# Kernel tuning notes

Measured on AMD Instinct MI355X. Metric: run time of the kernel, lower is better.

The kernel has to match this reference:

```python
import jax, jax.numpy as jnp
import numpy as np

B, N, M, C, H = 256, 4096, 64, 512, 4
IN, OUT = 64, 64
EPS = 1e-8

def setup_inputs():
    key = jax.random.key(0)
    ks = jax.random.split(key, 8)
    def w(k, shape, scale=0.05):
        return jax.random.normal(k, shape, dtype=jnp.float32) * scale
    return {
        "in_data": jax.random.normal(ks[0], (B, IN), dtype=jnp.float32),
        "memory": jax.random.normal(ks[1], (B, N, M), dtype=jnp.float32),
        "h0": jnp.zeros((B, C), jnp.float32),
        "c0": jnp.zeros((B, C), jnp.float32),
        "prev_weights": jnp.zeros((2 * H, B, N), jnp.float32),
        "prev_reads": jax.random.normal(ks[2], (H, B, M), dtype=jnp.float32),
        "W_ih": w(ks[3], (4 * C, IN + H * M)),
        "b_ih": jnp.zeros((4 * C,), jnp.float32),
        "W_hh": w(ks[4], (4 * C, C)),
        "b_hh": jnp.zeros((4 * C,), jnp.float32),
        "W_out": w(ks[5], (OUT, C + H * M)),
        "b_out": jnp.zeros((OUT,), jnp.float32),
        "W_addr": w(ks[6], (2 * H, M + 6, C)),
        "b_addr": jnp.zeros((2 * H, M + 6), jnp.float32),
        "W_ea": w(ks[7], (H, 2 * M, C)),
        "b_ea": jnp.zeros((H, 2 * M), jnp.float32),
    }


def reference(in_data, memory, h0, c0, prev_weights, prev_reads,
              W_ih, b_ih, W_hh, b_hh, W_out, b_out,
              W_addr, b_addr, W_ea, b_ea):
    # ---- controller: LSTMCell over [input, prev_reads...] ----
    x = jnp.concatenate([in_data] + [prev_reads[i] for i in range(H)], axis=-1)  # [B, IN+H*M]
    gates = x @ W_ih.T + b_ih + h0 @ W_hh.T + b_hh                               # [B, 4C]
    i_g, f_g, g_g, o_g = jnp.split(gates, 4, axis=-1)
    c = jax.nn.sigmoid(f_g) * c0 + jax.nn.sigmoid(i_g) * jnp.tanh(g_g)
    h = jax.nn.sigmoid(o_g) * jnp.tanh(c)

    # ---- heads: alternate read / write, sequential over memory ----
    mem = memory
    reads = []
    for hi in range(2 * H):
        p = c @ W_addr[hi].T + b_addr[hi]                     # [B, M+6]
        k = jnp.tanh(p[:, :M])                                # key
        beta = jax.nn.softplus(p[:, M:M + 1])                 # key strength
        gate = jax.nn.sigmoid(p[:, M + 1:M + 2])              # interpolation gate
        s = jax.nn.softmax(p[:, M + 2:M + 5], axis=-1)        # shift weights (3)
        gamma = 1.0 + jax.nn.softplus(p[:, M + 5:M + 6])      # sharpening
        # content addressing: cosine similarity against all memory rows
        dot = jnp.einsum('bnm,bm->bn', mem, k)                # [B, N]
        norms = jnp.linalg.norm(mem, axis=-1) * jnp.linalg.norm(k, axis=-1, keepdims=True)
        wc = jax.nn.softmax(beta * dot / (norms + EPS), axis=-1)
        # interpolation with previous weights
        wg = gate * wc + (1.0 - gate) * prev_weights[hi]
        # circular shift convolution (shifts -1, 0, +1)
        ws = (s[:, 0:1] * jnp.roll(wg, 1, axis=-1)
              + s[:, 1:2] * wg
              + s[:, 2:3] * jnp.roll(wg, -1, axis=-1))
        # sharpening
        wp = ws ** gamma
        w = wp / (jnp.sum(wp, axis=-1, keepdims=True) + EPS)
        if hi % 2 == 0:  # read head
            reads.append(jnp.einsum('bn,bnm->bm', w, mem))
        else:            # write head: erase then add
            ea = c @ W_ea[hi // 2].T + b_ea[hi // 2]          # [B, 2M]
            e = jax.nn.sigmoid(ea[:, :M])
            a = jnp.tanh(ea[:, M:])
            mem = mem * (1.0 - w[:, :, None] * e[:, None, :]) + w[:, :, None] * a[:, None, :]

    # ---- output layer over [h, reads...] ----
    state = jnp.concatenate([h] + reads, axis=-1)             # [B, C+H*M]
    return jax.nn.sigmoid(state @ W_out.T + b_out)            # [B, OUT]
```

## Files before the change

### kernel.cpp

```cpp
#include <hip/hip_runtime.h>
#include <hip/hip_fp16.h>
#include <math.h>

#define EPSF 1e-8f
#define NN 4096
#define BB 256
#define PH ((size_t)BB * NN)

__device__ __forceinline__ float sigf(float x) { return 1.0f / (1.0f + expf(-x)); }
__device__ __forceinline__ float softplusf(float x) { return x > 20.0f ? x : log1pf(expf(x)); }
__device__ __forceinline__ float dot4(float4 a, float4 b) {
  return a.x * b.x + a.y * b.y + a.z * b.z + a.w * b.w;
}
__device__ __forceinline__ unsigned short f2bf(float x) {
  unsigned int u = __float_as_uint(x);
  unsigned int r = (u + 0x7FFF + ((u >> 16) & 1)) >> 16;
  return (unsigned short)r;
}
__device__ __forceinline__ float bf2f(unsigned int lo16) {
  return __uint_as_float(lo16 << 16);
}

__device__ __forceinline__ float gather_x(const float* __restrict__ in_data,
                                          const float* __restrict__ prev_reads,
                                          const float* __restrict__ h0,
                                          int row, int k) {
  if (k < 64) return in_data[row * 64 + k];
  if (k < 320) { int i = (k - 64) >> 6, m = (k - 64) & 63; return prev_reads[((size_t)i * 256 + row) * 64 + m]; }
  return h0[row * 512 + (k - 320)];
}

__global__ __launch_bounds__(256) void gemm_gates_kernel(
    const float* __restrict__ in_data, const float* __restrict__ prev_reads,
    const float* __restrict__ h0, const float* __restrict__ W_ih,
    const float* __restrict__ W_hh, const float* __restrict__ b_ih,
    const float* __restrict__ b_hh, float* __restrict__ gates) {
  __shared__ float As[16][33];
  __shared__ float Ws[16][65];
  int tid = threadIdx.x, tx = tid & 15, ty = tid >> 4;
  int row0 = blockIdx.y * 32, col0 = blockIdx.x * 64;
  float acc[2][4] = {{0,0,0,0},{0,0,0,0}};
  for (int k0 = 0; k0 < 832; k0 += 16) {
    const float* Wp; int kw, KW;
    if (k0 < 320) { Wp = W_ih; kw = k0; KW = 320; }
    else          { Wp = W_hh; kw = k0 - 320; KW = 512; }
    for (int i = tid; i < 32 * 16; i += 256) {
      int rr = i >> 4, cc = i & 15;
      As[cc][rr] = gather_x(in_data, prev_reads, h0, row0 + rr, k0 + cc);
    }
    for (int i = tid; i < 64 * 16; i += 256) {
      int rr = i >> 4, cc = i & 15;
      Ws[cc][rr] = Wp[(size_t)(col0 + rr) * KW + kw + cc];
    }
    __syncthreads();
#pragma unroll
    for (int kk = 0; kk < 16; kk++) {
      float a0 = As[kk][ty * 2 + 0], a1 = As[kk][ty * 2 + 1];
      float w0 = Ws[kk][tx * 4 + 0], w1 = Ws[kk][tx * 4 + 1];
      float w2 = Ws[kk][tx * 4 + 2], w3 = Ws[kk][tx * 4 + 3];
      acc[0][0] += a0 * w0; acc[0][1] += a0 * w1; acc[0][2] += a0 * w2; acc[0][3] += a0 * w3;
      acc[1][0] += a1 * w0; acc[1][1] += a1 * w1; acc[1][2] += a1 * w2; acc[1][3] += a1 * w3;
    }
    __syncthreads();
  }
  for (int i = 0; i < 2; i++)
    for (int j = 0; j < 4; j++) {
      int cc = col0 + tx * 4 + j;
      gates[(size_t)(row0 + ty * 2 + i) * 2048 + cc] = acc[i][j] + b_ih[cc] + b_hh[cc];
    }
}

__global__ void lstm_elem_kernel(const float* __restrict__ gates,
                                 const float* __restrict__ c0,
                                 float* __restrict__ c, float* __restrict__ h) {
  int idx = blockIdx.x * 256 + threadIdx.x;
  if (idx >= 256 * 512) return;
  int b = idx >> 9, u = idx & 511;
  const float* g = gates + (size_t)b * 2048;
  float ig = sigf(g[u]), fg = sigf(g[512 + u]);
  float gg = tanhf(g[1024 + u]), og = sigf(g[1536 + u]);
  float cv = fg * c0[idx] + ig * gg;
  c[idx] = cv;
  h[idx] = og * tanhf(cv);
}

__global__ __launch_bounds__(256) void gemm_heads_kernel(
    const float* __restrict__ C, const float* __restrict__ W_addr,
    const float* __restrict__ W_ea, const float* __restrict__ b_addr,
    const float* __restrict__ b_ea, float* __restrict__ p_raw) {
  __shared__ float As[16][33];
  __shared__ float Ws[16][65];
  int tid = threadIdx.x, tx = tid & 15, ty = tid >> 4;
  int row0 = blockIdx.y * 32, col0 = blockIdx.x * 64;
  float acc[2][4] = {{0,0,0,0},{0,0,0,0}};
  for (int k0 = 0; k0 < 512; k0 += 16) {
    for (int i = tid; i < 32 * 16; i += 256) {
      int rr = i >> 4, cc = i & 15;
      As[cc][rr] = C[(size_t)(row0 + rr) * 512 + k0 + cc];
    }
    for (int i = tid; i < 64 * 16; i += 256) {
      int rr = i >> 4, cc = i & 15;
      int col = col0 + rr;
      float v = 0.f;
      if (col < 560) v = W_addr[(size_t)col * 512 + k0 + cc];
      else if (col < 1072) v = W_ea[(size_t)(col - 560) * 512 + k0 + cc];
      Ws[cc][rr] = v;
    }
    __syncthreads();
#pragma unroll
    for (int kk = 0; kk < 16; kk++) {
      float a0 = As[kk][ty * 2 + 0], a1 = As[kk][ty * 2 + 1];
      float w0 = Ws[kk][tx * 4 + 0], w1 = Ws[kk][tx * 4 + 1];
      float w2 = Ws[kk][tx * 4 + 2], w3 = Ws[kk][tx * 4 + 3];
      acc[0][0] += a0 * w0; acc[0][1] += a0 * w1; acc[0][2] += a0 * w2; acc[0][3] += a0 * w3;
      acc[1][0] += a1 * w0; acc[1][1] += a1 * w1; acc[1][2] += a1 * w2; acc[1][3] += a1 * w3;
    }
    __syncthreads();
  }
  for (int i = 0; i < 2; i++)
    for (int j = 0; j < 4; j++) {
      int col = col0 + tx * 4 + j;
      if (col < 1072) {
        float bias = col < 560 ? b_addr[col] : b_ea[col - 560];
        p_raw[(size_t)(row0 + ty * 2 + i) * 1072 + col] = acc[i][j] + bias;
      }
    }
}

__global__ void params_kernel(const float* __restrict__ p_raw,
    float* __restrict__ knorm, float* __restrict__ betav,
    float* __restrict__ gatev, float* __restrict__ sv,
    float* __restrict__ gammav, float* __restrict__ combo,
    float* __restrict__ scal) {
  int b = blockIdx.x, m = threadIdx.x;
  const float* p = p_raw + (size_t)b * 1072;
  float kv[7];
#pragma unroll
  for (int hi = 0; hi < 7; hi++) {
    float k = tanhf(p[hi * 70 + m]);
    kv[hi] = k;
    float s = k * k;
#pragma unroll
    for (int d = 1; d < 64; d <<= 1) s += __shfl_xor(s, d);
    if (m == 0) {
      int hb = hi * BB + b;
      knorm[hb] = sqrtf(s);
      betav[hb] = softplusf(p[hi * 70 + 64]);
      gatev[hb] = sigf(p[hi * 70 + 65]);
      float a0 = p[hi * 70 + 66], a1 = p[hi * 70 + 67], a2 = p[hi * 70 + 68];
      float mm = fmaxf(a0, fmaxf(a1, a2));
      float e0 = expf(a0 - mm), e1 = expf(a1 - mm), e2 = expf(a2 - mm);
      float es = e0 + e1 + e2;
      sv[hb * 3 + 0] = e0 / es; sv[hb * 3 + 1] = e1 / es; sv[hb * 3 + 2] = e2 / es;
      gammav[hb] = 1.0f + softplusf(p[hi * 70 + 69]);
    }
  }
  float e1 = sigf(p[560 + 0 * 128 + m]),  a1v = tanhf(p[560 + 0 * 128 + 64 + m]);
  float e3 = sigf(p[560 + 1 * 128 + m]),  a3v = tanhf(p[560 + 1 * 128 + 64 + m]);
  float e5 = sigf(p[560 + 2 * 128 + m]),  a5v = tanhf(p[560 + 2 * 128 + 64 + m]);
  size_t bm = (size_t)b * 64 + m;
  combo[0 * 16384 + bm] = kv[0];  combo[1 * 16384 + bm] = kv[1];
  combo[2 * 16384 + bm] = kv[2];  combo[3 * 16384 + bm] = e1 * kv[2];
  combo[4 * 16384 + bm] = kv[3];  combo[5 * 16384 + bm] = e1 * kv[3];
  combo[6 * 16384 + bm] = a1v;    combo[7 * 16384 + bm] = e1 * a1v;
  combo[8 * 16384 + bm] = e1;     combo[9 * 16384 + bm] = e1 * e1;
  combo[10 * 16384 + bm] = kv[4]; combo[11 * 16384 + bm] = kv[5];
  combo[12 * 16384 + bm] = kv[6]; combo[13 * 16384 + bm] = e5 * kv[6];
  combo[14 * 16384 + bm] = a5v;   combo[15 * 16384 + bm] = e5 * a5v;
  combo[16 * 16384 + bm] = e5;    combo[17 * 16384 + bm] = e5 * e5;
  combo[18 * 16384 + bm] = e3;    combo[19 * 16384 + bm] = a3v;
  float s0 = a1v * kv[2], s1 = a1v * kv[3], s2 = a1v * a1v, s3 = a5v * kv[6], s4 = a5v * a5v;
#pragma unroll
  for (int d = 1; d < 64; d <<= 1) {
    s0 += __shfl_xor(s0, d); s1 += __shfl_xor(s1, d); s2 += __shfl_xor(s2, d);
    s3 += __shfl_xor(s3, d); s4 += __shfl_xor(s4, d);
  }
  if (m == 0) {
    scal[b * 8 + 0] = s0; scal[b * 8 + 1] = s1; scal[b * 8 + 2] = s2;
    scal[b * 8 + 3] = s3; scal[b * 8 + 4] = s4;
  }
}

#define CL(j, q) (*(const float4*)(cb + (j) * 64 + (q) * 4))

__global__ __launch_bounds__(256) void phase1_kernel(
    const float* __restrict__ mem, const float* __restrict__ combo,
    const float* __restrict__ scal, const float* __restrict__ knorm,
    const float* __restrict__ betav, unsigned short* __restrict__ mem_bf,
    __half* __restrict__ P) {
  __shared__ float cb[640];
  __shared__ float4 tile[128 * 16];
  int b = blockIdx.y, tid = threadIdx.x;
  for (int i = tid; i < 640; i += 256)
    cb[i] = combo[(size_t)(i >> 6) * 16384 + b * 64 + (i & 63)];
  int n0 = blockIdx.x * 128;
  size_t bo = (size_t)b * NN;
  const float4* src = (const float4*)mem + (bo + n0) * 16;
  ushort4* dst = (ushort4*)mem_bf + (bo + n0) * 16;
#pragma unroll
  for (int i = 0; i < 8; i++) {
    int idx = tid + i * 256;
    float4 v = src[idx];
    int r = idx >> 4, q = idx & 15;
    tile[r * 16 + (q ^ (r & 15))] = v;
    ushort4 o;
    o.x = f2bf(v.x); o.y = f2bf(v.y); o.z = f2bf(v.z); o.w = f2bf(v.w);
    dst[idx] = o;
  }
  __syncthreads();
  float kn0 = knorm[b], be0 = betav[b];
  float kn1 = knorm[BB + b], be1 = betav[BB + b];
  float cak2 = scal[b * 8 + 0], cak3 = scal[b * 8 + 1], caa1 = scal[b * 8 + 2];
  int row = tid >> 1, half = tid & 1;
  float a[11];
#pragma unroll
  for (int k = 0; k < 11; k++) a[k] = 0.f;
#pragma unroll
  for (int j = 0; j < 8; j++) {
    int q = half * 8 + j;
    float4 v = tile[row * 16 + (q ^ (row & 15))];
    float4 sq = make_float4(v.x * v.x, v.y * v.y, v.z * v.z, v.w * v.w);
    a[0] += dot4(v, CL(0, q)); a[1] += dot4(v, CL(1, q));
    a[2] += dot4(v, CL(2, q)); a[3] += dot4(v, CL(3, q));
    a[4] += dot4(v, CL(4, q)); a[5] += dot4(v, CL(5, q));
    a[6] += dot4(v, CL(6, q)); a[7] += dot4(v, CL(7, q));
    a[8] += sq.x + sq.y + sq.z + sq.w;
    a[9] += dot4(sq, CL(8, q)); a[10] += dot4(sq, CL(9, q));
  }
#pragma unroll
  for (int k = 0; k < 11; k++) a[k] += __shfl_xor(a[k], 1);
  if (half == 0) {
    int n = n0 + row;
    float rn = sqrtf(a[8]);
    P[0 * PH + bo + n] = __float2half(be0 * a[0] / (rn * kn0 + EPSF));
    P[1 * PH + bo + n] = __float2half(be1 * a[1] / (rn * kn1 + EPSF));
    P[2 * PH + bo + n] = __float2half(a[2]);
    P[3 * PH + bo + n] = __float2half(a[3] - cak2);
    P[4 * PH + bo + n] = __float2half(a[4]);
    P[5 * PH + bo + n] = __float2half(a[5] - cak3);
    P[6 * PH + bo + n] = __float2half(a[8]);
    P[7 * PH + bo + n] = __float2half(a[9] - a[6]);
    P[8 * PH + bo + n] = __float2half(a[10] - 2.f * a[7] + caa1);
  }
}

__global__ __launch_bounds__(512) void chain_kernel(
    const __half* __restrict__ P, __half* __restrict__ w_g,
    const float* __restrict__ knorm, const float* __restrict__ betav,
    const float* __restrict__ gatev, const float* __restrict__ sv,
    const float* __restrict__ gammav, const float* __restrict__ prev_w,
    int group) {
  __shared__ float wg[NN];
  __shared__ float red[24];
  int b = blockIdx.x, hy = blockIdx.y, tid = threadIdx.x;
  int lane = tid & 63, wv = tid >> 6;
  int head, u_head = 0;
  const __half *SC = nullptr, *Da = nullptr, *Dbc = nullptr;
  const __half *S0p = nullptr, *T1p = nullptr, *T2p = nullptr;
  if (group == 0)      { head = hy;     SC = P + (size_t)hy * PH; }
  else if (group == 1) { head = 2 + hy; Da = P + (size_t)(2 + 2 * hy) * PH; Dbc = P + (size_t)(3 + 2 * hy) * PH;
                         S0p = P + 6 * PH; T1p = P + 7 * PH; T2p = P + 8 * PH; u_head = 1; }
  else if (group == 2) { head = 4 + hy; SC = P + (size_t)hy * PH; }
  else                 { head = 6;      Da = P + 2 * PH; Dbc = P + 3 * PH;
                         S0p = P + 4 * PH; T1p = P + 5 * PH; T2p = P + 6 * PH; u_head = 5; }
  int hb = head * BB + b;
  float kn = knorm[hb], be = betav[hb], ga = gatev[hb], gm = gammav[hb];
  float s0 = sv[hb * 3 + 0], s1 = sv[hb * 3 + 1], s2 = sv[hb * 3 + 2];
  size_t bo = (size_t)b * NN;
  const float* pw = prev_w + (size_t)head * PH + bo;
  const __half* ug = w_g + ((size_t)u_head * BB + b) * NN;
  __half* wout = w_g + ((size_t)head * BB + b) * NN;
  float sc[8];
  float mx = -1e30f;
#pragma unroll
  for (int i = 0; i < 8; i++) {
    int n = tid + i * 512;
    float scv;
    if (SC != nullptr) {
      scv = __half2float(SC[bo + n]);
    } else {
      float u = __half2float(ug[n]);
      float d = __half2float(Da[bo + n]) - u * __half2float(Dbc[bo + n]);
      float nn2 = __half2float(S0p[bo + n]) - 2.f * u * __half2float(T1p[bo + n])
                + u * u * __half2float(T2p[bo + n]);
      nn2 = fmaxf(nn2, 0.f);
      scv = be * d / (sqrtf(nn2) * kn + EPSF);
    }
    sc[i] = scv; mx = fmaxf(mx, scv);
  }
#pragma unroll
  for (int m = 1; m < 64; m <<= 1) mx = fmaxf(mx, __shfl_xor(mx, m));
  if (lane == 0) red[wv] = mx;
  __syncthreads();
  mx = red[0];
#pragma unroll
  for (int w = 1; w < 8; w++) mx = fmaxf(mx, red[w]);
  float sum = 0.f;
#pragma unroll
  for (int i = 0; i < 8; i++) { sc[i] = expf(sc[i] - mx); sum += sc[i]; }
#pragma unroll
  for (int m = 1; m < 64; m <<= 1) sum += __shfl_xor(sum, m);
  if (lane == 0) red[8 + wv] = sum;
  __syncthreads();
  sum = 0.f;
#pragma unroll
  for (int w = 0; w < 8; w++) sum += red[8 + w];
  float inv = 1.0f / sum;
#pragma unroll
  for (int i = 0; i < 8; i++) {
    int n = tid + i * 512;
    wg[n] = ga * (sc[i] * inv) + (1.f - ga) * pw[n];
  }
  __syncthreads();
  float wp[8];
  float sum2 = 0.f;
#pragma unroll
  for (int i = 0; i < 8; i++) {
    int n = tid + i * 512;
    float wsv = s0 * wg[(n + NN - 1) & (NN - 1)] + s1 * wg[n] + s2 * wg[(n + 1) & (NN - 1)];
    wp[i] = powf(wsv, gm);
    sum2 += wp[i];
  }
#pragma unroll
  for (int m = 1; m < 64; m <<= 1) sum2 += __shfl_xor(sum2, m);
  if (lane == 0) red[16 + wv] = sum2;
  __syncthreads();
  sum2 = 0.f;
#pragma unroll
  for (int w = 0; w < 8; w++) sum2 += red[16 + w];
  float invs = 1.0f / (sum2 + EPSF);
#pragma unroll
  for (int i = 0; i < 8; i++) {
    int n = tid + i * 512;
    wout[n] = __float2half(wp[i] * invs);
  }
}

__global__ __launch_bounds__(256) void phase2_kernel(
    const unsigned short* __restrict__ mem_bf, const float* __restrict__ combo,
    const float* __restrict__ scal, const float* __restrict__ knorm,
    const float* __restrict__ betav, const __half* __restrict__ w_g,
    __half* __restrict__ P) {
  __shared__ float cb[1280];
  __shared__ uint4 tileb[128 * 8];
  int b = blockIdx.y, tid = threadIdx.x;
  for (int i = tid; i < 1280; i += 256)
    cb[i] = combo[(size_t)(i >> 6) * 16384 + b * 64 + (i & 63)];
  int n0 = blockIdx.x * 128;
  size_t bo = (size_t)b * NN;
  const uint4* src = (const uint4*)mem_bf + (bo + n0) * 8;
#pragma unroll
  for (int i = 0; i < 4; i++) {
    int idx = tid + i * 256;
    uint4 u = src[idx];
    int r = idx >> 3, g = idx & 7;
    tileb[r * 8 + (g ^ (r & 7))] = u;
  }
  __syncthreads();
  float kn4 = knorm[4 * BB + b], be4 = betav[4 * BB + b];
  float kn5 = knorm[5 * BB + b], be5 = betav[5 * BB + b];
  float cak6 = scal[b * 8 + 3], caa5 = scal[b * 8 + 4];
  int row = tid >> 1, half = tid & 1;
  int n = n0 + row;
  float u1 = __half2float(w_g[((size_t)1 * BB + b) * NN + n]);
  float u3 = __half2float(w_g[((size_t)3 * BB + b) * NN + n]);
  float t[9];
#pragma unroll
  for (int k = 0; k < 9; k++) t[k] = 0.f;
#pragma unroll
  for (int j = 0; j < 4; j++) {
    int g = half * 4 + j;
    uint4 uv = tileb[row * 8 + (g ^ (row & 7))];
#pragma unroll
    for (int h = 0; h < 2; h++) {
      unsigned int pa = h ? uv.z : uv.x;
      unsigned int pb = h ? uv.w : uv.y;
      float4 v;
      v.x = bf2f(pa & 0xFFFFu); v.y = bf2f(pa >> 16);
      v.z = bf2f(pb & 0xFFFFu); v.w = bf2f(pb >> 16);
      int q = g * 2 + h;
      float4 e1v = CL(8, q), a1v = CL(6, q), e3v = CL(18, q), a3v = CL(19, q);
      float4 m1, m2;
      m1.x = v.x * (1.f - u1 * e1v.x) + u1 * a1v.x;
      m1.y = v.y * (1.f - u1 * e1v.y) + u1 * a1v.y;
      m1.z = v.z * (1.f - u1 * e1v.z) + u1 * a1v.z;
      m1.w = v.w * (1.f - u1 * e1v.w) + u1 * a1v.w;
      m2.x = m1.x * (1.f - u3 * e3v.x) + u3 * a3v.x;
      m2.y = m1.y * (1.f - u3 * e3v.y) + u3 * a3v.y;
      m2.z = m1.z * (1.f - u3 * e3v.z) + u3 * a3v.z;
      m2.w = m1.w * (1.f - u3 * e3v.w) + u3 * a3v.w;
      float4 sq = make_float4(m2.x * m2.x, m2.y * m2.y, m2.z * m2.z, m2.w * m2.w);
      t[0] += dot4(m2, CL(10, q)); t[1] += dot4(m2, CL(11, q));
      t[2] += dot4(m2, CL(12, q)); t[3] += dot4(m2, CL(13, q));
      t[4] += dot4(m2, CL(14, q)); t[5] += dot4(m2, CL(15, q));
      t[6] += sq.x + sq.y + sq.z + sq.w;
      t[7] += dot4(sq, CL(16, q)); t[8] += dot4(sq, CL(17, q));
    }
  }
#pragma unroll
  for (int k = 0; k < 9; k++) t[k] += __shfl_xor(t[k], 1);
  if (half == 0) {
    float rn = sqrtf(t[6]);
    P[0 * PH + bo + n] = __float2half(be4 * t[0] / (rn * kn4 + EPSF));
    P[1 * PH + bo + n] = __float2half(be5 * t[1] / (rn * kn5 + EPSF));
    P[2 * PH + bo + n] = __float2half(t[2]);
    P[3 * PH + bo + n] = __float2half(t[3] - cak6);
    P[4 * PH + bo + n] = __float2half(t[6]);
    P[5 * PH + bo + n] = __float2half(t[7] - t[4]);
    P[6 * PH + bo + n] = __float2half(t[8] - 2.f * t[5] + caa5);
  }
}

__global__ __launch_bounds__(256) void phase3_kernel(
    const unsigned short* __restrict__ mem_bf, const float* __restrict__ combo,
    const __half* __restrict__ w_g, float* __restrict__ reads) {
  __shared__ float cb[1280];
  __shared__ __half ws[7 * 512];
  __shared__ float sred[4 * 4 * 16 * 4];
  int b = blockIdx.y, chunk = blockIdx.x, tid = threadIdx.x;
  for (int i = tid; i < 1280; i += 256)
    cb[i] = combo[(size_t)(i >> 6) * 16384 + b * 64 + (i & 63)];
  int nbase = chunk * 512;
  for (int i = tid; i < 7 * 512; i += 256) {
    int hh = i >> 9, nn = i & 511;
    ws[i] = w_g[((size_t)hh * BB + b) * NN + nbase + nn];
  }
  __syncthreads();
  int wv = tid >> 6, lane = tid & 63, q = lane & 15, rl = lane >> 4;
  float4 e1v = CL(8, q), a1v = CL(6, q), e3v = CL(18, q), a3v = CL(19, q);
  float4 e5v = CL(16, q), a5v = CL(14, q);
  size_t bo = (size_t)b * NN;
  const ushort4* mbr = (const ushort4*)mem_bf + bo * 16;
  float A[4][4];
#pragma unroll
  for (int j = 0; j < 4; j++)
#pragma unroll
    for (int cmp = 0; cmp < 4; cmp++) A[j][cmp] = 0.f;
#pragma unroll 4
  for (int t = 0; t < 32; t++) {
    int nl = t * 16 + wv * 4 + rl;
    int n = nbase + nl;
    ushort4 uv = mbr[(size_t)n * 16 + q];
    float vx = bf2f(uv.x), vy = bf2f(uv.y), vz = bf2f(uv.z), vw = bf2f(uv.w);
    float w0v = __half2float(ws[0 * 512 + nl]);
    float u1  = __half2float(ws[1 * 512 + nl]);
    float w2v = __half2float(ws[2 * 512 + nl]);
    float u3  = __half2float(ws[3 * 512 + nl]);
    float w4v = __half2float(ws[4 * 512 + nl]);
    float u5  = __half2float(ws[5 * 512 + nl]);
    float w6v = __half2float(ws[6 * 512 + nl]);
    A[0][0] += w0v * vx; A[0][1] += w0v * vy; A[0][2] += w0v * vz; A[0][3] += w0v * vw;
    float m1x = vx * (1.f - u1 * e1v.x) + u1 * a1v.x;
    float m1y = vy * (1.f - u1 * e1v.y) + u1 * a1v.y;
    float m1z = vz * (1.f - u1 * e1v.z) + u1 * a1v.z;
    float m1w = vw * (1.f - u1 * e1v.w) + u1 * a1v.w;
    A[1][0] += w2v * m1x; A[1][1] += w2v * m1y; A[1][2] += w2v * m1z; A[1][3] += w2v * m1w;
    float m2x = m1x * (1.f - u3 * e3v.x) + u3 * a3v.x;
    float m2y = m1y * (1.f - u3 * e3v.y) + u3 * a3v.y;
    float m2z = m1z * (1.f - u3 * e3v.z) + u3 * a3v.z;
    float m2w = m1w * (1.f - u3 * e3v.w) + u3 * a3v.w;
    A[2][0] += w4v * m2x; A[2][1] += w4v * m2y; A[2][2] += w4v * m2z; A[2][3] += w4v * m2w;
    float m3x = m2x * (1.f - u5 * e5v.x) + u5 * a5v.x;
    float m3y = m2y * (1.f - u5 * e5v.y) + u5 * a5v.y;
    float m3z = m2z * (1.f - u5 * e5v.z) + u5 * a5v.z;
    float m3w = m2w * (1.f - u5 * e5v.w) + u5 * a5v.w;
    A[3][0] += w6v * m3x; A[3][1] += w6v * m3y; A[3][2] += w6v * m3z; A[3][3] += w6v * m3w;
  }
#pragma unroll
  for (int j = 0; j < 4; j++)
#pragma unroll
    for (int cmp = 0; cmp < 4; cmp++) {
      float x = A[j][cmp];
      x += __shfl_xor(x, 16);
      x += __shfl_xor(x, 32);
      A[j][cmp] = x;
    }
  if (rl == 0)
#pragma unroll
    for (int j = 0; j < 4; j++)
#pragma unroll
      for (int cmp = 0; cmp < 4; cmp++)
        sred[((j * 4 + wv) * 16 + q) * 4 + cmp] = A[j][cmp];
  __syncthreads();
  if (tid < 256) {
    int j = tid >> 6, qq = (tid >> 2) & 15, cc = tid & 3;
    float s = 0.f;
#pragma unroll
    for (int w = 0; w < 4; w++) s += sred[((j * 4 + w) * 16 + qq) * 4 + cc];
    atomicAdd(&reads[(size_t)j * 16384 + b * 64 + qq * 4 + cc], s);
  }
}

__global__ __launch_bounds__(256) void gemm_out_kernel(
    const float* __restrict__ h, const float* __restrict__ reads,
    const float* __restrict__ W_out, const float* __restrict__ b_out,
    float* __restrict__ out) {
  __shared__ float As[16][33];
  __shared__ float Ws[16][65];
  int tid = threadIdx.x, tx = tid & 15, ty = tid >> 4;
  int row0 = blockIdx.y * 32;
  float acc[2][4] = {{0,0,0,0},{0,0,0,0}};
  for (int k0 = 0; k0 < 768; k0 += 16) {
    for (int i = tid; i < 32 * 16; i += 256) {
      int rr = i >> 4, cc = i & 15;
      int row = row0 + rr, k = k0 + cc;
      float v;
      if (k < 512) v = h[row * 512 + k];
      else { int slot = (k - 512) >> 6, m = (k - 512) & 63; v = reads[((size_t)slot * 256 + row) * 64 + m]; }
      As[cc][rr] = v;
    }
    for (int i = tid; i < 64 * 16; i += 256) {
      int rr = i >> 4, cc = i & 15;
      Ws[cc][rr] = W_out[(size_t)rr * 768 + k0 + cc];
    }
    __syncthreads();
#pragma unroll
    for (int kk = 0; kk < 16; kk++) {
      float a0 = As[kk][ty * 2 + 0], a1 = As[kk][ty * 2 + 1];
      float w0 = Ws[kk][tx * 4 + 0], w1 = Ws[kk][tx * 4 + 1];
      float w2 = Ws[kk][tx * 4 + 2], w3 = Ws[kk][tx * 4 + 3];
      acc[0][0] += a0 * w0; acc[0][1] += a0 * w1; acc[0][2] += a0 * w2; acc[0][3] += a0 * w3;
      acc[1][0] += a1 * w0; acc[1][1] += a1 * w1; acc[1][2] += a1 * w2; acc[1][3] += a1 * w3;
    }
    __syncthreads();
  }
  for (int i = 0; i < 2; i++)
    for (int j = 0; j < 4; j++) {
      int cc = tx * 4 + j;
      out[(size_t)(row0 + ty * 2 + i) * 64 + cc] = sigf(acc[i][j] + b_out[cc]);
    }
}

extern "C" void kernel_launch(void* const* d_in, const int* in_sizes, int n_in,
                              void* d_out, int out_size, void* d_ws, size_t ws_size,
                              hipStream_t stream) {
  const float* in_data = (const float*)d_in[0];
  const float* memory  = (const float*)d_in[1];
  const float* h0      = (const float*)d_in[2];
  const float* c0      = (const float*)d_in[3];
  const float* prev_w  = (const float*)d_in[4];
  const float* prev_r  = (const float*)d_in[5];
  const float* W_ih    = (const float*)d_in[6];
  const float* b_ih    = (const float*)d_in[7];
  const float* W_hh    = (const float*)d_in[8];
  const float* b_hh    = (const float*)d_in[9];
  const float* W_out   = (const float*)d_in[10];
  const float* b_out   = (const float*)d_in[11];
  const float* W_addr  = (const float*)d_in[12];
  const float* b_addr  = (const float*)d_in[13];
  const float* W_ea    = (const float*)d_in[14];
  const float* b_ea    = (const float*)d_in[15];
  float* out = (float*)d_out;
  (void)in_sizes; (void)n_in; (void)out_size; (void)ws_size;

  float* ws = (float*)d_ws;
  size_t off = 0;
  auto alloc = [&](size_t n) { float* p = ws + off; off += (n + 63) & ~(size_t)63; return p; };
  float* gates  = alloc(256 * 2048);
  float* cbuf   = alloc(256 * 512);
  float* hbuf   = alloc(256 * 512);
  float* p_raw  = alloc(256 * 1072);
  float* knorm  = alloc(8 * 256);
  float* betav  = alloc(8 * 256);
  float* gatev  = alloc(8 * 256);
  float* sv     = alloc(8 * 256 * 3);
  float* gammav = alloc(8 * 256);
  float* combo  = alloc(20 * 16384);
  float* scal   = alloc(256 * 8);
  __half* P     = (__half*)alloc(9 * PH / 2);
  float* reads  = alloc(4 * 16384);
  unsigned short* mem_bf = (unsigned short*)alloc(33554432);
  __half* w_g   = (__half*)alloc(7 * BB * NN / 2);

  gemm_gates_kernel<<<dim3(32, 8), 256, 0, stream>>>(in_data, prev_r, h0, W_ih, W_hh, b_ih, b_hh, gates);
  lstm_elem_kernel<<<(256 * 512 + 255) / 256, 256, 0, stream>>>(gates, c0, cbuf, hbuf);
  gemm_heads_kernel<<<dim3(17, 8), 256, 0, stream>>>(cbuf, W_addr, W_ea, b_addr, b_ea, p_raw);
  params_kernel<<<256, 64, 0, stream>>>(p_raw, knorm, betav, gatev, sv, gammav, combo, scal);
  hipMemsetAsync(reads, 0, 4 * 16384 * sizeof(float), stream);

  phase1_kernel<<<dim3(32, 256), 256, 0, stream>>>(memory, combo, scal, knorm, betav, mem_bf, P);
  chain_kernel<<<dim3(256, 2), 512, 0, stream>>>(P, w_g, knorm, betav, gatev, sv, gammav, prev_w, 0);
  chain_kernel<<<dim3(256, 2), 512, 0, stream>>>(P, w_g, knorm, betav, gatev, sv, gammav, prev_w, 1);
  phase2_kernel<<<dim3(32, 256), 256, 0, stream>>>(mem_bf, combo, scal, knorm, betav, w_g, P);
  chain_kernel<<<dim3(256, 2), 512, 0, stream>>>(P, w_g, knorm, betav, gatev, sv, gammav, prev_w, 2);
  chain_kernel<<<dim3(256, 1), 512, 0, stream>>>(P, w_g, knorm, betav, gatev, sv, gammav, prev_w, 3);
  phase3_kernel<<<dim3(8, 256), 256, 0, stream>>>(mem_bf, combo, w_g, reads);

  gemm_out_kernel<<<dim3(1, 8), 256, 0, stream>>>(hbuf, reads, W_out, b_out, out);
}
```

Before: 888.1 us.

## Merge front-end and chain kernels using software grid barriers

Fuses the gate GEMM, LSTM elementwise, heads GEMM and params stages into one persistent 256-block kernel. Pairs of chain kernels are merged into two kernels separated by atomic grid-wide barriers, which removes several launch gaps. Also switches expf/powf to the fast __expf/__powf intrinsics in the chain. The barriers assume all blocks are co-resident and can deadlock otherwise; the chain23 second stage idles half the blocks, and the fast intrinsics are slightly less accurate.

```diff
diff --git a/kernel.cpp b/kernel.cpp
--- a/kernel.cpp
+++ b/kernel.cpp
@@ -19,6 +19,21 @@
 }
 __device__ __forceinline__ float bf2f(unsigned int lo16) {
   return __uint_as_float(lo16 << 16);
+}
+
+__device__ __forceinline__ void gbar(unsigned* arr, unsigned* rel, unsigned nb, unsigned call) {
+  __syncthreads();
+  if (threadIdx.x == 0) {
+    unsigned old = __hip_atomic_fetch_add(arr, 1u, __ATOMIC_ACQ_REL, __HIP_MEMORY_SCOPE_AGENT);
+    if (old == call * nb - 1u) {
+      __hip_atomic_store(rel, call, __ATOMIC_RELEASE, __HIP_MEMORY_SCOPE_AGENT);
+    } else {
+      while (__hip_atomic_load(rel, __ATOMIC_ACQUIRE, __HIP_MEMORY_SCOPE_AGENT) < call) {
+        __builtin_amdgcn_s_sleep(2);
+      }
+    }
+  }
+  __syncthreads();
 }
 
 __device__ __forceinline__ float gather_x(const float* __restrict__ in_data,
@@ -30,154 +45,159 @@
   return h0[row * 512 + (k - 320)];
 }
 
-__global__ __launch_bounds__(256) void gemm_gates_kernel(
+__global__ __launch_bounds__(256) void front_kernel(
     const float* __restrict__ in_data, const float* __restrict__ prev_reads,
-    const float* __restrict__ h0, const float* __restrict__ W_ih,
-    const float* __restrict__ W_hh, const float* __restrict__ b_ih,
-    const float* __restrict__ b_hh, float* __restrict__ gates) {
-  __shared__ float As[16][33];
-  __shared__ float Ws[16][65];
-  int tid = threadIdx.x, tx = tid & 15, ty = tid >> 4;
-  int row0 = blockIdx.y * 32, col0 = blockIdx.x * 64;
-  float acc[2][4] = {{0,0,0,0},{0,0,0,0}};
-  for (int k0 = 0; k0 < 832; k0 += 16) {
-    const float* Wp; int kw, KW;
-    if (k0 < 320) { Wp = W_ih; kw = k0; KW = 320; }
-    else          { Wp = W_hh; kw = k0 - 320; KW = 512; }
-    for (int i = tid; i < 32 * 16; i += 256) {
-      int rr = i >> 4, cc = i & 15;
-      As[cc][rr] = gather_x(in_data, prev_reads, h0, row0 + rr, k0 + cc);
-    }
-    for (int i = tid; i < 64 * 16; i += 256) {
-      int rr = i >> 4, cc = i & 15;
-      Ws[cc][rr] = Wp[(size_t)(col0 + rr) * KW + kw + cc];
-    }
-    __syncthreads();
-#pragma unroll
-    for (int kk = 0; kk < 16; kk++) {
-      float a0 = As[kk][ty * 2 + 0], a1 = As[kk][ty * 2 + 1];
-      float w0 = Ws[kk][tx * 4 + 0], w1 = Ws[kk][tx * 4 + 1];
-      float w2 = Ws[kk][tx * 4 + 2], w3 = Ws[kk][tx * 4 + 3];
-      acc[0][0] += a0 * w0; acc[0][1] += a0 * w1; acc[0][2] += a0 * w2; acc[0][3] += a0 * w3;
-      acc[1][0] += a1 * w0; acc[1][1] += a1 * w1; acc[1][2] += a1 * w2; acc[1][3] += a1 * w3;
-    }
-    __syncthreads();
-  }
-  for (int i = 0; i < 2; i++)
-    for (int j = 0; j < 4; j++) {
-      int cc = col0 + tx * 4 + j;
-      gates[(size_t)(row0 + ty * 2 + i) * 2048 + cc] = acc[i][j] + b_ih[cc] + b_hh[cc];
-    }
-}
-
-__global__ void lstm_elem_kernel(const float* __restrict__ gates,
-                                 const float* __restrict__ c0,
-                                 float* __restrict__ c, float* __restrict__ h) {
-  int idx = blockIdx.x * 256 + threadIdx.x;
-  if (idx >= 256 * 512) return;
-  int b = idx >> 9, u = idx & 511;
-  const float* g = gates + (size_t)b * 2048;
-  float ig = sigf(g[u]), fg = sigf(g[512 + u]);
-  float gg = tanhf(g[1024 + u]), og = sigf(g[1536 + u]);
-  float cv = fg * c0[idx] + ig * gg;
-  c[idx] = cv;
-  h[idx] = og * tanhf(cv);
-}
-
-__global__ __launch_bounds__(256) void gemm_heads_kernel(
-    const float* __restrict__ C, const float* __restrict__ W_addr,
-    const float* __restrict__ W_ea, const float* __restrict__ b_addr,
-    const float* __restrict__ b_ea, float* __restrict__ p_raw) {
-  __shared__ float As[16][33];
-  __shared__ float Ws[16][65];
-  int tid = threadIdx.x, tx = tid & 15, ty = tid >> 4;
-  int row0 = blockIdx.y * 32, col0 = blockIdx.x * 64;
-  float acc[2][4] = {{0,0,0,0},{0,0,0,0}};
-  for (int k0 = 0; k0 < 512; k0 += 16) {
-    for (int i = tid; i < 32 * 16; i += 256) {
-      int rr = i >> 4, cc = i & 15;
-      As[cc][rr] = C[(size_t)(row0 + rr) * 512 + k0 + cc];
-    }
-    for (int i = tid; i < 64 * 16; i += 256) {
-      int rr = i >> 4, cc = i & 15;
-      int col = col0 + rr;
-      float v = 0.f;
-      if (col < 560) v = W_addr[(size_t)col * 512 + k0 + cc];
-      else if (col < 1072) v = W_ea[(size_t)(col - 560) * 512 + k0 + cc];
-      Ws[cc][rr] = v;
-    }
-    __syncthreads();
-#pragma unroll
-    for (int kk = 0; kk < 16; kk++) {
-      float a0 = As[kk][ty * 2 + 0], a1 = As[kk][ty * 2 + 1];
-      float w0 = Ws[kk][tx * 4 + 0], w1 = Ws[kk][tx * 4 + 1];
-      float w2 = Ws[kk][tx * 4 + 2], w3 = Ws[kk][tx * 4 + 3];
-      acc[0][0] += a0 * w0; acc[0][1] += a0 * w1; acc[0][2] += a0 * w2; acc[0][3] += a0 * w3;
-      acc[1][0] += a1 * w0; acc[1][1] += a1 * w1; acc[1][2] += a1 * w2; acc[1][3] += a1 * w3;
-    }
-    __syncthreads();
-  }
-  for (int i = 0; i < 2; i++)
-    for (int j = 0; j < 4; j++) {
-      int col = col0 + tx * 4 + j;
-      if (col < 1072) {
-        float bias = col < 560 ? b_addr[col] : b_ea[col - 560];
-        p_raw[(size_t)(row0 + ty * 2 + i) * 1072 + col] = acc[i][j] + bias;
-      }
-    }
-}
-
-__global__ void params_kernel(const float* __restrict__ p_raw,
+    const float* __restrict__ h0, const float* __restrict__ c0,
+    const float* __restrict__ W_ih, const float* __restrict__ W_hh,
+    const float* __restrict__ b_ih, const float* __restrict__ b_hh,
+    const float* __restrict__ W_addr, const float* __restrict__ W_ea,
+    const float* __restrict__ b_addr, const float* __restrict__ b_ea,
+    float* __restrict__ gates, float* __restrict__ cbuf, float* __restrict__ hbuf,
+    float* __restrict__ p_raw,
     float* __restrict__ knorm, float* __restrict__ betav,
     float* __restrict__ gatev, float* __restrict__ sv,
     float* __restrict__ gammav, float* __restrict__ combo,
-    float* __restrict__ scal) {
-  int b = blockIdx.x, m = threadIdx.x;
-  const float* p = p_raw + (size_t)b * 1072;
-  float kv[7];
-#pragma unroll
-  for (int hi = 0; hi < 7; hi++) {
-    float k = tanhf(p[hi * 70 + m]);
-    kv[hi] = k;
-    float s = k * k;
-#pragma unroll
-    for (int d = 1; d < 64; d <<= 1) s += __shfl_xor(s, d);
+    float* __restrict__ scal, unsigned* __restrict__ bars) {
+  __shared__ float As[16][33];
+  __shared__ float Ws[16][65];
+  int tid = threadIdx.x, blk = blockIdx.x;
+  int tx = tid & 15, ty = tid >> 4;
+
+  {
+    int col0 = (blk & 31) * 64, row0 = (blk >> 5) * 32;
+    float acc[2][4] = {{0,0,0,0},{0,0,0,0}};
+    for (int k0 = 0; k0 < 832; k0 += 16) {
+      const float* Wp; int kw, KW;
+      if (k0 < 320) { Wp = W_ih; kw = k0; KW = 320; }
+      else          { Wp = W_hh; kw = k0 - 320; KW = 512; }
+      for (int i = tid; i < 32 * 16; i += 256) {
+        int rr = i >> 4, cc = i & 15;
+        As[cc][rr] = gather_x(in_data, prev_reads, h0, row0 + rr, k0 + cc);
+      }
+      for (int i = tid; i < 64 * 16; i += 256) {
+        int rr = i >> 4, cc = i & 15;
+        Ws[cc][rr] = Wp[(size_t)(col0 + rr) * KW + kw + cc];
+      }
+      __syncthreads();
+#pragma unroll
+      for (int kk = 0; kk < 16; kk++) {
+        float a0 = As[kk][ty * 2 + 0], a1 = As[kk][ty * 2 + 1];
+        float w0 = Ws[kk][tx * 4 + 0], w1 = Ws[kk][tx * 4 + 1];
+        float w2 = Ws[kk][tx * 4 + 2], w3 = Ws[kk][tx * 4 + 3];
+        acc[0][0] += a0 * w0; acc[0][1] += a0 * w1; acc[0][2] += a0 * w2; acc[0][3] += a0 * w3;
+        acc[1][0] += a1 * w0; acc[1][1] += a1 * w1; acc[1][2] += a1 * w2; acc[1][3] += a1 * w3;
+      }
+      __syncthreads();
+    }
+    for (int i = 0; i < 2; i++)
+      for (int j = 0; j < 4; j++) {
+        int cc = col0 + tx * 4 + j;
+        gates[(size_t)(row0 + ty * 2 + i) * 2048 + cc] = acc[i][j] + b_ih[cc] + b_hh[cc];
+      }
+  }
+  gbar(bars + 0, bars + 1, 256, 1);
+
+  {
+#pragma unroll
+    for (int r = 0; r < 2; r++) {
+      int idx = blk * 512 + r * 256 + tid;
+      int b = idx >> 9, u = idx & 511;
+      const float* g = gates + (size_t)b * 2048;
+      float ig = sigf(g[u]), fg = sigf(g[512 + u]);
+      float gg = tanhf(g[1024 + u]), og = sigf(g[1536 + u]);
+      float cv = fg * c0[idx] + ig * gg;
+      cbuf[idx] = cv;
+      hbuf[idx] = og * tanhf(cv);
+    }
+  }
+  gbar(bars + 0, bars + 1, 256, 2);
+
+  if (blk < 136) {
+    int col0 = (blk % 17) * 64, row0 = (blk / 17) * 32;
+    float acc[2][4] = {{0,0,0,0},{0,0,0,0}};
+    for (int k0 = 0; k0 < 512; k0 += 16) {
+      for (int i = tid; i < 32 * 16; i += 256) {
+        int rr = i >> 4, cc = i & 15;
+        As[cc][rr] = cbuf[(size_t)(row0 + rr) * 512 + k0 + cc];
+      }
+      for (int i = tid; i < 64 * 16; i += 256) {
+        int rr = i >> 4, cc = i & 15;
+        int col = col0 + rr;
+        float v = 0.f;
+        if (col < 560) v = W_addr[(size_t)col * 512 + k0 + cc];
+        else if (col < 1072) v = W_ea[(size_t)(col - 560) * 512 + k0 + cc];
+        Ws[cc][rr] = v;
+      }
+      __syncthreads();
+#pragma unroll
+      for (int kk = 0; kk < 16; kk++) {
+        float a0 = As[kk][ty * 2 + 0], a1 = As[kk][ty * 2 + 1];
+        float w0 = Ws[kk][tx * 4 + 0], w1 = Ws[kk][tx * 4 + 1];
+        float w2 = Ws[kk][tx * 4 + 2], w3 = Ws[kk][tx * 4 + 3];
+        acc[0][0] += a0 * w0; acc[0][1] += a0 * w1; acc[0][2] += a0 * w2; acc[0][3] += a0 * w3;
+        acc[1][0] += a1 * w0; acc[1][1] += a1 * w1; acc[1][2] += a1 * w2; acc[1][3] += a1 * w3;
+      }
+      __syncthreads();
+    }
+    for (int i = 0; i < 2; i++)
+      for (int j = 0; j < 4; j++) {
+        int col = col0 + tx * 4 + j;
+        if (col < 1072) {
+          float bias = col < 560 ? b_addr[col] : b_ea[col - 560];
+          p_raw[(size_t)(row0 + ty * 2 + i) * 1072 + col] = acc[i][j] + bias;
+        }
+      }
+  }
+  gbar(bars + 0, bars + 1, 256, 3);
+
+  if (tid < 64) {
+    int b = blk, m = tid;
+    const float* p = p_raw + (size_t)b * 1072;
+    float kv[7];
+#pragma unroll
+    for (int hi = 0; hi < 7; hi++) {
+      float k = tanhf(p[hi * 70 + m]);
+      kv[hi] = k;
+      float s = k * k;
+#pragma unroll
+      for (int d = 1; d < 64; d <<= 1) s += __shfl_xor(s, d);
+      if (m == 0) {
+        int hb = hi * BB + b;
+        knorm[hb] = sqrtf(s);
+        betav[hb] = softplusf(p[hi * 70 + 64]);
+        gatev[hb] = sigf(p[hi * 70 + 65]);
+        float a0 = p[hi * 70 + 66], a1 = p[hi * 70 + 67], a2 = p[hi * 70 + 68];
+        float mm = fmaxf(a0, fmaxf(a1, a2));
+        float e0 = expf(a0 - mm), e1 = expf(a1 - mm), e2 = expf(a2 - mm);
+        float es = e0 + e1 + e2;
+        sv[hb * 3 + 0] = e0 / es; sv[hb * 3 + 1] = e1 / es; sv[hb * 3 + 2] = e2 / es;
+        gammav[hb] = 1.0f + softplusf(p[hi * 70 + 69]);
+      }
+    }
+    float e1 = sigf(p[560 + 0 * 128 + m]),  a1v = tanhf(p[560 + 0 * 128 + 64 + m]);
+    float e3 = sigf(p[560 + 1 * 128 + m]),  a3v = tanhf(p[560 + 1 * 128 + 64 + m]);
+    float e5 = sigf(p[560 + 2 * 128 + m]),  a5v = tanhf(p[560 + 2 * 128 + 64 + m]);
+    size_t bm = (size_t)b * 64 + m;
+    combo[0 * 16384 + bm] = kv[0];  combo[1 * 16384 + bm] = kv[1];
+    combo[2 * 16384 + bm] = kv[2];  combo[3 * 16384 + bm] = e1 * kv[2];
+    combo[4 * 16384 + bm] = kv[3];  combo[5 * 16384 + bm] = e1 * kv[3];
+    combo[6 * 16384 + bm] = a1v;    combo[7 * 16384 + bm] = e1 * a1v;
+    combo[8 * 16384 + bm] = e1;     combo[9 * 16384 + bm] = e1 * e1;
+    combo[10 * 16384 + bm] = kv[4]; combo[11 * 16384 + bm] = kv[5];
+    combo[12 * 16384 + bm] = kv[6]; combo[13 * 16384 + bm] = e5 * kv[6];
+    combo[14 * 16384 + bm] = a5v;   combo[15 * 16384 + bm] = e5 * a5v;
+    combo[16 * 16384 + bm] = e5;    combo[17 * 16384 + bm] = e5 * e5;
+    combo[18 * 16384 + bm] = e3;    combo[19 * 16384 + bm] = a3v;
+    float s0 = a1v * kv[2], s1 = a1v * kv[3], s2 = a1v * a1v, s3 = a5v * kv[6], s4 = a5v * a5v;
+#pragma unroll
+    for (int d = 1; d < 64; d <<= 1) {
+      s0 += __shfl_xor(s0, d); s1 += __shfl_xor(s1, d); s2 += __shfl_xor(s2, d);
+      s3 += __shfl_xor(s3, d); s4 += __shfl_xor(s4, d);
+    }
     if (m == 0) {
-      int hb = hi * BB + b;
-      knorm[hb] = sqrtf(s);
-      betav[hb] = softplusf(p[hi * 70 + 64]);
-      gatev[hb] = sigf(p[hi * 70 + 65]);
-      float a0 = p[hi * 70 + 66], a1 = p[hi * 70 + 67], a2 = p[hi * 70 + 68];
-      float mm = fmaxf(a0, fmaxf(a1, a2));
-      float e0 = expf(a0 - mm), e1 = expf(a1 - mm), e2 = expf(a2 - mm);
-      float es = e0 + e1 + e2;
-      sv[hb * 3 + 0] = e0 / es; sv[hb * 3 + 1] = e1 / es; sv[hb * 3 + 2] = e2 / es;
-      gammav[hb] = 1.0f + softplusf(p[hi * 70 + 69]);
-    }
-  }
-  float e1 = sigf(p[560 + 0 * 128 + m]),  a1v = tanhf(p[560 + 0 * 128 + 64 + m]);
-  float e3 = sigf(p[560 + 1 * 128 + m]),  a3v = tanhf(p[560 + 1 * 128 + 64 + m]);
-  float e5 = sigf(p[560 + 2 * 128 + m]),  a5v = tanhf(p[560 + 2 * 128 + 64 + m]);
-  size_t bm = (size_t)b * 64 + m;
-  combo[0 * 16384 + bm] = kv[0];  combo[1 * 16384 + bm] = kv[1];
-  combo[2 * 16384 + bm] = kv[2];  combo[3 * 16384 + bm] = e1 * kv[2];
-  combo[4 * 16384 + bm] = kv[3];  combo[5 * 16384 + bm] = e1 * kv[3];
-  combo[6 * 16384 + bm] = a1v;    combo[7 * 16384 + bm] = e1 * a1v;
-  combo[8 * 16384 + bm] = e1;     combo[9 * 16384 + bm] = e1 * e1;
-  combo[10 * 16384 + bm] = kv[4]; combo[11 * 16384 + bm] = kv[5];
-  combo[12 * 16384 + bm] = kv[6]; combo[13 * 16384 + bm] = e5 * kv[6];
-  combo[14 * 16384 + bm] = a5v;   combo[15 * 16384 + bm] = e5 * a5v;
-  combo[16 * 16384 + bm] = e5;    combo[17 * 16384 + bm] = e5 * e5;
-  combo[18 * 16384 + bm] = e3;    combo[19 * 16384 + bm] = a3v;
-  float s0 = a1v * kv[2], s1 = a1v * kv[3], s2 = a1v * a1v, s3 = a5v * kv[6], s4 = a5v * a5v;
-#pragma unroll
-  for (int d = 1; d < 64; d <<= 1) {
-    s0 += __shfl_xor(s0, d); s1 += __shfl_xor(s1, d); s2 += __shfl_xor(s2, d);
-    s3 += __shfl_xor(s3, d); s4 += __shfl_xor(s4, d);
-  }
-  if (m == 0) {
-    scal[b * 8 + 0] = s0; scal[b * 8 + 1] = s1; scal[b * 8 + 2] = s2;
-    scal[b * 8 + 3] = s3; scal[b * 8 + 4] = s4;
+      scal[b * 8 + 0] = s0; scal[b * 8 + 1] = s1; scal[b * 8 + 2] = s2;
+      scal[b * 8 + 3] = s3; scal[b * 8 + 4] = s4;
+    }
   }
 }
 
@@ -244,32 +264,21 @@
   }
 }
 
-__global__ __launch_bounds__(512) void chain_kernel(
-    const __half* __restrict__ P, __half* __restrict__ w_g,
+__device__ void chain_core(int tid, int b, int head,
+    const __half* __restrict__ SC, const __half* __restrict__ Da,
+    const __half* __restrict__ Dbc, const __half* __restrict__ S0p,
+    const __half* __restrict__ T1p, const __half* __restrict__ T2p,
+    const __half* __restrict__ ug, __half* __restrict__ wout,
+    float* wg, float* red,
     const float* __restrict__ knorm, const float* __restrict__ betav,
     const float* __restrict__ gatev, const float* __restrict__ sv,
-    const float* __restrict__ gammav, const float* __restrict__ prev_w,
-    int group) {
-  __shared__ float wg[NN];
-  __shared__ float red[24];
-  int b = blockIdx.x, hy = blockIdx.y, tid = threadIdx.x;
+    const float* __restrict__ gammav, const float* __restrict__ prev_w) {
   int lane = tid & 63, wv = tid >> 6;
-  int head, u_head = 0;
-  const __half *SC = nullptr, *Da = nullptr, *Dbc = nullptr;
-  const __half *S0p = nullptr, *T1p = nullptr, *T2p = nullptr;
-  if (group == 0)      { head = hy;     SC = P + (size_t)hy * PH; }
-  else if (group == 1) { head = 2 + hy; Da = P + (size_t)(2 + 2 * hy) * PH; Dbc = P + (size_t)(3 + 2 * hy) * PH;
-                         S0p = P + 6 * PH; T1p = P + 7 * PH; T2p = P + 8 * PH; u_head = 1; }
-  else if (group == 2) { head = 4 + hy; SC = P + (size_t)hy * PH; }
-  else                 { head = 6;      Da = P + 2 * PH; Dbc = P + 3 * PH;
-                         S0p = P + 4 * PH; T1p = P + 5 * PH; T2p = P + 6 * PH; u_head = 5; }
   int hb = head * BB + b;
   float kn = knorm[hb], be = betav[hb], ga = gatev[hb], gm = gammav[hb];
   float s0 = sv[hb * 3 + 0], s1 = sv[hb * 3 + 1], s2 = sv[hb * 3 + 2];
   size_t bo = (size_t)b * NN;
   const float* pw = prev_w + (size_t)head * PH + bo;
-  const __half* ug = w_g + ((size_t)u_head * BB + b) * NN;
-  __half* wout = w_g + ((size_t)head * BB + b) * NN;
   float sc[8];
   float mx = -1e30f;
 #pragma unroll
@@ -297,7 +306,7 @@
   for (int w = 1; w < 8; w++) mx = fmaxf(mx, red[w]);
   float sum = 0.f;
 #pragma unroll
-  for (int i = 0; i < 8; i++) { sc[i] = expf(sc[i] - mx); sum += sc[i]; }
+  for (int i = 0; i < 8; i++) { sc[i] = __expf(sc[i] - mx); sum += sc[i]; }
 #pragma unroll
   for (int m = 1; m < 64; m <<= 1) sum += __shfl_xor(sum, m);
   if (lane == 0) red[8 + wv] = sum;
@@ -318,7 +327,7 @@
   for (int i = 0; i < 8; i++) {
     int n = tid + i * 512;
     float wsv = s0 * wg[(n + NN - 1) & (NN - 1)] + s1 * wg[n] + s2 * wg[(n + 1) & (NN - 1)];
-    wp[i] = powf(wsv, gm);
+    wp[i] = __powf(wsv, gm);
     sum2 += wp[i];
   }
 #pragma unroll
@@ -333,6 +342,48 @@
   for (int i = 0; i < 8; i++) {
     int n = tid + i * 512;
     wout[n] = __float2half(wp[i] * invs);
+  }
+  __syncthreads();
+}
+
+__global__ __launch_bounds__(512) void chains01_kernel(
+    const __half* __restrict__ P, __half* __restrict__ w_g,
+    const float* __restrict__ knorm, const float* __restrict__ betav,
+    const float* __restrict__ gatev, const float* __restrict__ sv,
+    const float* __restrict__ gammav, const float* __restrict__ prev_w,
+    unsigned* __restrict__ bars) {
+  __shared__ float wg[NN];
+  __shared__ float red[24];
+  int b = blockIdx.x, hy = blockIdx.y, tid = threadIdx.x;
+  chain_core(tid, b, hy, P + (size_t)hy * PH, nullptr, nullptr, nullptr, nullptr, nullptr,
+             nullptr, w_g + ((size_t)hy * BB + b) * NN, wg, red,
+             knorm, betav, gatev, sv, gammav, prev_w);
+  gbar(bars + 0, bars + 1, 512, 1);
+  chain_core(tid, b, 2 + hy, nullptr,
+             P + (size_t)(2 + 2 * hy) * PH, P + (size_t)(3 + 2 * hy) * PH,
+             P + 6 * PH, P + 7 * PH, P + 8 * PH,
+             w_g + ((size_t)1 * BB + b) * NN, w_g + ((size_t)(2 + hy) * BB + b) * NN, wg, red,
+             knorm, betav, gatev, sv, gammav, prev_w);
+}
+
+__global__ __launch_bounds__(512) void chains23_kernel(
+    const __half* __restrict__ P, __half* __restrict__ w_g,
+    const float* __restrict__ knorm, const float* __restrict__ betav,
+    const float* __restrict__ gatev, const float* __restrict__ sv,
+    const float* __restrict__ gammav, const float* __restrict__ prev_w,
+    unsigned* __restrict__ bars) {
+  __shared__ float wg[NN];
+  __shared__ float red[24];
+  int b = blockIdx.x, hy = blockIdx.y, tid = threadIdx.x;
+  chain_core(tid, b, 4 + hy, P + (size_t)hy * PH, nullptr, nullptr, nullptr, nullptr, nullptr,
+             nullptr, w_g + ((size_t)(4 + hy) * BB + b) * NN, wg, red,
+             knorm, betav, gatev, sv, gammav, prev_w);
+  gbar(bars + 0, bars + 1, 512, 1);
+  if (hy == 0) {
+    chain_core(tid, b, 6, nullptr, P + 2 * PH, P + 3 * PH,
+               P + 4 * PH, P + 5 * PH, P + 6 * PH,
+               w_g + ((size_t)5 * BB + b) * NN, w_g + ((size_t)6 * BB + b) * NN, wg, red,
+               knorm, betav, gatev, sv, gammav, prev_w);
   }
 }
 
@@ -569,22 +620,21 @@
   float* scal   = alloc(256 * 8);
   __half* P     = (__half*)alloc(9 * PH / 2);
   float* reads  = alloc(4 * 16384);
+  unsigned* bars = (unsigned*)alloc(64);
   unsigned short* mem_bf = (unsigned short*)alloc(33554432);
   __half* w_g   = (__half*)alloc(7 * BB * NN / 2);
 
-  gemm_gates_kernel<<<dim3(32, 8), 256, 0, stream>>>(in_data, prev_r, h0, W_ih, W_hh, b_ih, b_hh, gates);
-  lstm_elem_kernel<<<(256 * 512 + 255) / 256, 256, 0, stream>>>(gates, c0, cbuf, hbuf);
-  gemm_heads_kernel<<<dim3(17, 8), 256, 0, stream>>>(cbuf, W_addr, W_ea, b_addr, b_ea, p_raw);
-  params_kernel<<<256, 64, 0, stream>>>(p_raw, knorm, betav, gatev, sv, gammav, combo, scal);
-  hipMemsetAsync(reads, 0, 4 * 16384 * sizeof(float), stream);
-
+  (void)hipMemsetAsync(reads, 0, (4 * 16384 + 64) * sizeof(float), stream);
+
+  front_kernel<<<256, 256, 0, stream>>>(in_data, prev_r, h0, c0, W_ih, W_hh, b_ih, b_hh,
+                                        W_addr, W_ea, b_addr, b_ea,
+                                        gates, cbuf, hbuf, p_raw,
+                                        knorm, betav, gatev, sv, gammav, combo, scal,
+                                        bars + 0);
   phase1_kernel<<<dim3(32, 256), 256, 0, stream>>>(memory, combo, scal, knorm, betav, mem_bf, P);
-  chain_kernel<<<dim3(256, 2), 512, 0, stream>>>(P, w_g, knorm, betav, gatev, sv, gammav, prev_w, 0);
-  chain_kernel<<<dim3(256, 2), 512, 0, stream>>>(P, w_g, knorm, betav, gatev, sv, gammav, prev_w, 1);
+  chains01_kernel<<<dim3(256, 2), 512, 0, stream>>>(P, w_g, knorm, betav, gatev, sv, gammav, prev_w, bars + 2);
   phase2_kernel<<<dim3(32, 256), 256, 0, stream>>>(mem_bf, combo, scal, knorm, betav, w_g, P);
-  chain_kernel<<<dim3(256, 2), 512, 0, stream>>>(P, w_g, knorm, betav, gatev, sv, gammav, prev_w, 2);
-  chain_kernel<<<dim3(256, 1), 512, 0, stream>>>(P, w_g, knorm, betav, gatev, sv, gammav, prev_w, 3);
+  chains23_kernel<<<dim3(256, 2), 512, 0, stream>>>(P, w_g, knorm, betav, gatev, sv, gammav, prev_w, bars + 4);
   phase3_kernel<<<dim3(8, 256), 256, 0, stream>>>(mem_bf, combo, w_g, reads);
-
   gemm_out_kernel<<<dim3(1, 8), 256, 0, stream>>>(hbuf, reads, W_out, b_out, out);
 }
```

Measured after the change: 1.087 ms. 1.22x slower.
